# Kernel tuning notes

Hardware: AMD Instinct MI355X
Metric: run time of the kernel (lower is better)

Reference implementation:

```python
import jax, jax.numpy as jnp
import numpy as np

D_MODEL = 768
NUM_HEADS = 12
D_HEAD = D_MODEL // NUM_HEADS


def setup_inputs() -> dict:
    key = jax.random.key(0)
    ks = jax.random.split(key, 11)
    B, S = 1, 4096
    s = 1.0 / np.sqrt(D_MODEL)
    inp = {
        'q': jax.random.normal(ks[0], (B, S, D_MODEL), dtype=jnp.float32),
        'k': jax.random.normal(ks[1], (B, S, D_MODEL), dtype=jnp.float32),
        'v': jax.random.normal(ks[2], (B, S, D_MODEL), dtype=jnp.float32),
        'wq': jax.random.normal(ks[3], (D_MODEL, D_MODEL), dtype=jnp.float32) * s,
        'bq': jnp.zeros((D_MODEL,), dtype=jnp.float32),
        'wk': jax.random.normal(ks[4], (D_MODEL, D_MODEL), dtype=jnp.float32) * s,
        'bk': jnp.zeros((D_MODEL,), dtype=jnp.float32),
        'wv': jax.random.normal(ks[5], (D_MODEL, D_MODEL), dtype=jnp.float32) * s,
        'bv': jnp.zeros((D_MODEL,), dtype=jnp.float32),
        'wo': jax.random.normal(ks[6], (D_MODEL, D_MODEL), dtype=jnp.float32) * s,
        'bo': jnp.zeros((D_MODEL,), dtype=jnp.float32),
    }
    return inp


def reference(q, k, v, wq, bq, wk, bk, wv, bv, wo, bo):
    B, S, _ = q.shape
    # linear projections (torch Linear: x @ W^T + b)
    qh = (q @ wq.T + bq).reshape(B, S, NUM_HEADS, D_HEAD).transpose(0, 2, 1, 3)
    kh = (k @ wk.T + bk).reshape(B, S, NUM_HEADS, D_HEAD).transpose(0, 2, 1, 3)
    vh = (v @ wv.T + bv).reshape(B, S, NUM_HEADS, D_HEAD).transpose(0, 2, 1, 3)
    scores = jnp.einsum('bhqd,bhkd->bhqk', qh, kh) / jnp.sqrt(jnp.float32(D_HEAD))
    causal = jnp.tril(jnp.ones((S, S), dtype=bool))  # [S,S] causal mask
    scores = jnp.where(causal, scores, jnp.finfo(scores.dtype).min)
    attn = jax.nn.softmax(scores, axis=-1)  # dropout omitted (eval mode)
    out = jnp.einsum('bhqk,bhkd->bhqd', attn, vh)
    out = out.transpose(0, 2, 1, 3).reshape(B, S, D_MODEL)
    return out @ wo.T + bo
```

## Files before the change

### kernel.cpp

```cpp
#include <hip/hip_runtime.h>
#include <stdint.h>

typedef __attribute__((ext_vector_type(8))) short short8;
typedef __attribute__((ext_vector_type(4))) short short4v;
typedef __attribute__((ext_vector_type(4))) float float4v;
typedef __attribute__((ext_vector_type(2))) uint32_t uint32x2;
typedef __attribute__((ext_vector_type(4))) uint32_t uint32x4;

__device__ __forceinline__ unsigned short f2bf(float f) {
  union { float f; uint32_t u; } v;
  v.f = f;
  uint32_t u = v.u;
  return (unsigned short)((u + 0x7fffu + ((u >> 16) & 1u)) >> 16);
}

__device__ __forceinline__ uint32_t pkbf(float a, float b) {
#if __has_builtin(__builtin_amdgcn_cvt_pk_bf16_f32)
  typedef __attribute__((ext_vector_type(2))) __bf16 bf16x2;
  bf16x2 r = __builtin_amdgcn_cvt_pk_bf16_f32(a, b);
  union { bf16x2 v; uint32_t u; } c;
  c.v = r;
  return c.u;
#else
  return (uint32_t)f2bf(a) | ((uint32_t)f2bf(b) << 16);
#endif
}

__device__ __forceinline__ float fexp2(float x) {
#if __has_builtin(__builtin_amdgcn_exp2f)
  return __builtin_amdgcn_exp2f(x);
#else
  return exp2f(x);
#endif
}

__device__ __forceinline__ float4v mfma16bf(short4v a, short4v b, float4v c) {
#if __has_builtin(__builtin_amdgcn_mfma_f32_16x16x16bf16_1k)
  return __builtin_amdgcn_mfma_f32_16x16x16bf16_1k(a, b, c, 0, 0, 0);
#else
  float4v d;
  asm("v_mfma_f32_16x16x16_bf16 %0, %1, %2, %3"
      : "=v"(d) : "v"(a), "v"(b), "v"(c));
  return d;
#endif
}

__device__ __forceinline__ void gll16(const unsigned short* g, unsigned short* l) {
  __builtin_amdgcn_global_load_lds(
      (const __attribute__((address_space(1))) void*)g,
      (__attribute__((address_space(3))) void*)l, 16, 0, 0);
}

struct CvtArgs {
  const float* src[4];
  unsigned short* dst[4];
};

__global__ __launch_bounds__(256) void cvt_all(CvtArgs a) {
  const int bid = blockIdx.x;
  const int t = bid / 288, off = bid - t * 288;
  const size_t i = (size_t)off * 256 + threadIdx.x;
  const float4v* p = (const float4v*)(a.src[t] + i * 8);
  float4v x = p[0], y = p[1];
  uint32x4 o;
  o[0] = pkbf(x[0], x[1]);
  o[1] = pkbf(x[2], x[3]);
  o[2] = pkbf(y[0], y[1]);
  o[3] = pkbf(y[2], y[3]);
  *(uint32x4*)(a.dst[t] + i * 8) = o;
}

__global__ __launch_bounds__(256) void gemm_qkv(
    const float* __restrict__ xq, const float* __restrict__ xk,
    const float* __restrict__ xv,
    const unsigned short* __restrict__ wqb, const unsigned short* __restrict__ wkb,
    const unsigned short* __restrict__ wvb,
    const float* __restrict__ bq, const float* __restrict__ bk,
    const float* __restrict__ bv,
    unsigned short* __restrict__ Qp, unsigned short* __restrict__ Kp,
    unsigned short* __restrict__ Vt, float qscale)
{
  __shared__ unsigned short As[128 * 64];
  __shared__ unsigned short Ws[128 * 64];
  const int z = blockIdx.z;
  const float* A32 = z == 0 ? xq : z == 1 ? xk : xv;
  const unsigned short* W = z == 0 ? wqb : z == 1 ? wkb : wvb;
  const float* bias = z == 0 ? bq : z == 1 ? bk : bv;
  const int M = 4096, N = 768, K = 768;
  const int tid = threadIdx.x, wave = tid >> 6, lane = tid & 63;
  const int g = lane >> 4, l16 = lane & 15;
  const int sw = l16 & 7;
  const int m0 = blockIdx.x * 128, n0 = blockIdx.y * 128;
  const int wn = (wave >> 1) * 64, wm = (wave & 1) * 64;
  const int srow0 = wave * 32 + (lane >> 3);
  const int skg = lane & 7;

  float4v acc[4][4] = {};

  for (int k0 = 0; k0 < K; k0 += 64) {
    if (k0) __syncthreads();
    #pragma unroll
    for (int c = 0; c < 4; ++c) {
      const int row = srow0 + c * 8;
      const int kg = skg ^ (row & 7);
      gll16(W + (size_t)(n0 + row) * K + k0 + kg * 8, &Ws[(wave * 32 + c * 8) * 64]);
    }
    #pragma unroll
    for (int inst = 0; inst < 8; ++inst) {
      const int f = inst * 256 + tid;
      const int row = f >> 4, c = f & 15;
      float4v a = *(const float4v*)(A32 + (size_t)(m0 + row) * K + k0 + c * 4);
      uint32x2 pk;
      pk[0] = pkbf(a[0], a[1]);
      pk[1] = pkbf(a[2], a[3]);
      const int s = c >> 1;
      *(uint32x2*)&As[row * 64 + ((s ^ (row & 7)) * 8) + (c & 1) * 4] = pk;
    }
    __syncthreads();
    #pragma unroll
    for (int kk = 0; kk < 2; ++kk) {
      const int kg = ((kk * 4 + g) ^ sw) * 8;
      short8 xf[4], wf[4];
      #pragma unroll
      for (int t = 0; t < 4; ++t) {
        xf[t] = *(const short8*)&As[(wm + t * 16 + l16) * 64 + kg];
        wf[t] = *(const short8*)&Ws[(wn + t * 16 + l16) * 64 + kg];
      }
      if (z < 2) {
        #pragma unroll
        for (int i = 0; i < 4; ++i)
          #pragma unroll
          for (int j = 0; j < 4; ++j)
            acc[i][j] = __builtin_amdgcn_mfma_f32_16x16x32_bf16(wf[i], xf[j], acc[i][j], 0, 0, 0);
      } else {
        #pragma unroll
        for (int i = 0; i < 4; ++i)
          #pragma unroll
          for (int j = 0; j < 4; ++j)
            acc[i][j] = __builtin_amdgcn_mfma_f32_16x16x32_bf16(xf[i], wf[j], acc[i][j], 0, 0, 0);
      }
    }
  }

  if (z < 2) {
    unsigned short* O = z == 0 ? Qp : Kp;
    const float osc = z == 0 ? qscale : 1.0f;
    #pragma unroll
    for (int i = 0; i < 4; ++i) {
      const int nb = n0 + wn + i * 16 + 4 * g;
      const float4v bb = *(const float4v*)&bias[nb];
      #pragma unroll
      for (int j = 0; j < 4; ++j) {
        const int m = m0 + wm + j * 16 + l16;
        uint32x2 pk;
        pk[0] = pkbf((acc[i][j][0] + bb[0]) * osc, (acc[i][j][1] + bb[1]) * osc);
        pk[1] = pkbf((acc[i][j][2] + bb[2]) * osc, (acc[i][j][3] + bb[3]) * osc);
        *(uint32x2*)(O + (size_t)m * N + nb) = pk;
      }
    }
  } else {
    #pragma unroll
    for (int j = 0; j < 4; ++j) {
      const int n = n0 + wn + j * 16 + l16;
      const float bb = bias[n];
      #pragma unroll
      for (int i = 0; i < 4; ++i) {
        const int mb = m0 + wm + i * 16 + 4 * g;
        uint32x2 pk;
        pk[0] = pkbf(acc[i][j][0] + bb, acc[i][j][1] + bb);
        pk[1] = pkbf(acc[i][j][2] + bb, acc[i][j][3] + bb);
        *(uint32x2*)(Vt + (size_t)n * M + mb) = pk;
      }
    }
  }
}

__global__ __launch_bounds__(256, 4) void flash_part(
    const unsigned short* __restrict__ Qp,
    const unsigned short* __restrict__ Kp,
    const unsigned short* __restrict__ Vt,
    unsigned short* __restrict__ Opart,
    float* __restrict__ lpart)
{
  __shared__ unsigned short lds_k[2][64 * 64];
  __shared__ unsigned short lds_v[2][64 * 64];
  const int S = 4096, DM = 768;

  const int gid = blockIdx.x;
  const int h = gid % 12;
  const int e = 79 - gid / 12;
  int t, c;
  if (e < 8)       { t = e;                c = 0; }
  else if (e < 24) { t = 8 + (e - 8) / 2;  c = (e - 8) % 2; }
  else if (e < 48) { t = 16 + (e - 24) / 3; c = (e - 24) % 3; }
  else             { t = 24 + (e - 48) / 4; c = (e - 48) % 4; }
  const int kb0 = c * 16;
  const int kbe = min(kb0 + 16, 2 * t + 2);

  const int tid = threadIdx.x, wave = tid >> 6, lane = tid & 63;
  const int g = lane >> 4, l16 = lane & 15;
  const int sw = l16 & 7;
  const int qbase = t * 128 + wave * 32;

  short8 qf[2][2];
  #pragma unroll
  for (int qc = 0; qc < 2; ++qc) {
    const unsigned short* qp = Qp + (size_t)(qbase + qc * 16 + l16) * DM + h * 64;
    qf[qc][0] = *(const short8*)(qp + g * 8);
    qf[qc][1] = *(const short8*)(qp + 32 + g * 8);
  }

  float4v o[2][4] = {};
  float lsum[2] = {0.0f, 0.0f};

  const int strow = wave * 16 + (lane >> 3);
  const int skg = lane & 7;

  #pragma unroll
  for (int cc = 0; cc < 2; ++cc) {
    const int row = strow + cc * 8;
    const int kg = skg ^ (row & 7);
    gll16(Kp + (size_t)(kb0 * 64 + row) * DM + h * 64 + kg * 8,
          &lds_k[0][(wave * 16 + cc * 8) * 64]);
    gll16(Vt + (size_t)(h * 64 + row) * S + kb0 * 64 + kg * 8,
          &lds_v[0][(wave * 16 + cc * 8) * 64]);
  }
  __syncthreads();

  for (int kb = kb0; kb < kbe; ++kb) {
    const int cur = kb & 1;
    if (kb + 1 < kbe) {
      const int nb = cur ^ 1;
      #pragma unroll
      for (int cc = 0; cc < 2; ++cc) {
        const int row = strow + cc * 8;
        const int kg = skg ^ (row & 7);
        gll16(Kp + (size_t)((kb + 1) * 64 + row) * DM + h * 64 + kg * 8,
              &lds_k[nb][(wave * 16 + cc * 8) * 64]);
        gll16(Vt + (size_t)(h * 64 + row) * S + (kb + 1) * 64 + kg * 8,
              &lds_v[nb][(wave * 16 + cc * 8) * 64]);
      }
    }
    const unsigned short* kc = lds_k[cur];
    const unsigned short* vc = lds_v[cur];

    float4v sf[2][4];
    #pragma unroll
    for (int mt = 0; mt < 4; ++mt) {
      short8 ka0 = *(const short8*)&kc[(mt * 16 + l16) * 64 + ((0 + g) ^ sw) * 8];
      short8 ka1 = *(const short8*)&kc[(mt * 16 + l16) * 64 + ((4 + g) ^ sw) * 8];
      #pragma unroll
      for (int qc = 0; qc < 2; ++qc) {
        float4v a = {};
        a = __builtin_amdgcn_mfma_f32_16x16x32_bf16(ka0, qf[qc][0], a, 0, 0, 0);
        a = __builtin_amdgcn_mfma_f32_16x16x32_bf16(ka1, qf[qc][1], a, 0, 0, 0);
        sf[qc][mt] = a;
      }
    }

    if ((kb + 1) * 64 > qbase) {
      #pragma unroll
      for (int qc = 0; qc < 2; ++qc) {
        const int q = qbase + qc * 16 + l16;
        #pragma unroll
        for (int mt = 0; mt < 4; ++mt)
          #pragma unroll
          for (int rr = 0; rr < 4; ++rr) {
            const int key = kb * 64 + mt * 16 + 4 * g + rr;
            sf[qc][mt][rr] = (key <= q) ? sf[qc][mt][rr] : -1e30f;
          }
      }
    }

    short4v pb[2][4];
    #pragma unroll
    for (int qc = 0; qc < 2; ++qc)
      #pragma unroll
      for (int mt = 0; mt < 4; ++mt) {
        float4v pe;
        #pragma unroll
        for (int rr = 0; rr < 4; ++rr) {
          pe[rr] = fexp2(sf[qc][mt][rr]);
          lsum[qc] += pe[rr];
        }
        union { uint32x2 u; short4v s; } cv;
        cv.u[0] = pkbf(pe[0], pe[1]);
        cv.u[1] = pkbf(pe[2], pe[3]);
        pb[qc][mt] = cv.s;
      }

    #pragma unroll
    for (int ms = 0; ms < 4; ++ms) {
      const int slot = ((2 * ms + (g >> 1)) ^ sw) * 8 + (g & 1) * 4;
      #pragma unroll
      for (int dt = 0; dt < 4; ++dt) {
        short4v va = *(const short4v*)&vc[(dt * 16 + l16) * 64 + slot];
        o[0][dt] = mfma16bf(va, pb[0][ms], o[0][dt]);
        o[1][dt] = mfma16bf(va, pb[1][ms], o[1][dt]);
      }
    }

    __syncthreads();
  }

  const int slot = (h * 32 + t) * 4 + c;
  unsigned short* ob = Opart + (size_t)slot * 8192;
  #pragma unroll
  for (int qc = 0; qc < 2; ++qc) {
    float L = lsum[qc];
    L += __shfl_xor(L, 16);
    L += __shfl_xor(L, 32);
    const int ql = wave * 32 + qc * 16 + l16;
    if (g == 0) lpart[slot * 128 + ql] = L;
    #pragma unroll
    for (int dt = 0; dt < 4; ++dt) {
      uint32x2 ov;
      ov[0] = pkbf(o[qc][dt][0], o[qc][dt][1]);
      ov[1] = pkbf(o[qc][dt][2], o[qc][dt][3]);
      *(uint32x2*)(ob + (size_t)ql * 64 + dt * 16 + 4 * g) = ov;
    }
  }
}

__global__ __launch_bounds__(256) void flash_combine(
    const unsigned short* __restrict__ Opart, const float* __restrict__ lpart,
    unsigned short* __restrict__ AO)
{
  const int t = blockIdx.x, h = blockIdx.y;
  const int nc = (2 * t + 17) >> 4;
  const int slot0 = (h * 32 + t) * 4;
  const int tid = threadIdx.x;
  const int qr = tid >> 2, dc = (tid & 3) * 16;
  #pragma unroll
  for (int it = 0; it < 2; ++it) {
    const int ql = it * 64 + qr;
    float acc[16];
    #pragma unroll
    for (int j = 0; j < 16; ++j) acc[j] = 0.0f;
    float lsum = 0.0f;
    for (int cc = 0; cc < nc; ++cc) {
      const int slot = slot0 + cc;
      lsum += lpart[slot * 128 + ql];
      const uint32x4* p = (const uint32x4*)(Opart + (size_t)slot * 8192 + ql * 64 + dc);
      uint32x4 w0 = p[0], w1 = p[1];
      #pragma unroll
      for (int j = 0; j < 4; ++j) {
        union { uint32_t u; float f; } lo, hi;
        lo.u = w0[j] << 16; hi.u = w0[j] & 0xffff0000u;
        acc[2 * j] += lo.f; acc[2 * j + 1] += hi.f;
        lo.u = w1[j] << 16; hi.u = w1[j] & 0xffff0000u;
        acc[8 + 2 * j] += lo.f; acc[8 + 2 * j + 1] += hi.f;
      }
    }
    const float inv = 1.0f / lsum;
    uint32x4 o0, o1;
    #pragma unroll
    for (int j = 0; j < 4; ++j) {
      o0[j] = pkbf(acc[2 * j] * inv, acc[2 * j + 1] * inv);
      o1[j] = pkbf(acc[8 + 2 * j] * inv, acc[8 + 2 * j + 1] * inv);
    }
    unsigned short* dst = AO + (size_t)(t * 128 + ql) * 768 + h * 64 + dc;
    *(uint32x4*)dst = o0;
    *(uint32x4*)(dst + 8) = o1;
  }
}

__global__ __launch_bounds__(256) void gemm_out(
    const unsigned short* __restrict__ A, const unsigned short* __restrict__ W,
    const float* __restrict__ bias, float* __restrict__ Out)
{
  __shared__ unsigned short As[128 * 64];
  __shared__ unsigned short Ws[128 * 64];
  const int N = 768, K = 768;
  const int tid = threadIdx.x, wave = tid >> 6, lane = tid & 63;
  const int g = lane >> 4, l16 = lane & 15;
  const int sw = l16 & 7;
  const int m0 = blockIdx.x * 128, n0 = blockIdx.y * 128;
  const int wn = (wave >> 1) * 64, wm = (wave & 1) * 64;
  const int srow0 = wave * 32 + (lane >> 3);
  const int skg = lane & 7;

  float4v acc[4][4] = {};

  for (int k0 = 0; k0 < K; k0 += 64) {
    if (k0) __syncthreads();
    #pragma unroll
    for (int c = 0; c < 4; ++c) {
      const int row = srow0 + c * 8;
      const int kg = skg ^ (row & 7);
      gll16(A + (size_t)(m0 + row) * K + k0 + kg * 8, &As[(wave * 32 + c * 8) * 64]);
      gll16(W + (size_t)(n0 + row) * K + k0 + kg * 8, &Ws[(wave * 32 + c * 8) * 64]);
    }
    __syncthreads();
    #pragma unroll
    for (int kk = 0; kk < 2; ++kk) {
      const int kg = ((kk * 4 + g) ^ sw) * 8;
      short8 xf[4], wf[4];
      #pragma unroll
      for (int t = 0; t < 4; ++t) {
        xf[t] = *(const short8*)&As[(wm + t * 16 + l16) * 64 + kg];
        wf[t] = *(const short8*)&Ws[(wn + t * 16 + l16) * 64 + kg];
      }
      #pragma unroll
      for (int i = 0; i < 4; ++i)
        #pragma unroll
        for (int j = 0; j < 4; ++j)
          acc[i][j] = __builtin_amdgcn_mfma_f32_16x16x32_bf16(wf[i], xf[j], acc[i][j], 0, 0, 0);
    }
  }

  #pragma unroll
  for (int i = 0; i < 4; ++i) {
    const int nb = n0 + wn + i * 16 + 4 * g;
    const float4v bb = *(const float4v*)&bias[nb];
    #pragma unroll
    for (int j = 0; j < 4; ++j) {
      const int m = m0 + wm + j * 16 + l16;
      float4v ov;
      #pragma unroll
      for (int rr = 0; rr < 4; ++rr) ov[rr] = acc[i][j][rr] + bb[rr];
      *(float4v*)(Out + (size_t)m * N + nb) = ov;
    }
  }
}

extern "C" void kernel_launch(void* const* d_in, const int* in_sizes, int n_in,
                              void* d_out, int out_size, void* d_ws, size_t ws_size,
                              hipStream_t stream) {
  const float* q  = (const float*)d_in[0];
  const float* k  = (const float*)d_in[1];
  const float* v  = (const float*)d_in[2];
  const float* wq = (const float*)d_in[3];
  const float* bq = (const float*)d_in[4];
  const float* wk = (const float*)d_in[5];
  const float* bk = (const float*)d_in[6];
  const float* wv = (const float*)d_in[7];
  const float* bv = (const float*)d_in[8];
  const float* wo = (const float*)d_in[9];
  const float* bo = (const float*)d_in[10];
  float* out = (float*)d_out;

  const int S = 4096, D = 768;
  unsigned short* Qp    = (unsigned short*)d_ws;
  unsigned short* Kp    = Qp  + (size_t)S * D;
  unsigned short* Vt    = Kp  + (size_t)S * D;
  unsigned short* AO    = Vt  + (size_t)S * D;
  unsigned short* wqb   = AO  + (size_t)S * D;
  unsigned short* wkb   = wqb + (size_t)D * D;
  unsigned short* wvb   = wkb + (size_t)D * D;
  unsigned short* wob   = wvb + (size_t)D * D;
  unsigned short* Opart = wob + (size_t)D * D;
  float*          lpart = (float*)(Opart + (size_t)1536 * 8192);

  CvtArgs ca;
  ca.src[0] = wq; ca.dst[0] = wqb;
  ca.src[1] = wk; ca.dst[1] = wkb;
  ca.src[2] = wv; ca.dst[2] = wvb;
  ca.src[3] = wo; ca.dst[3] = wob;

  const float SC = 0.125f * 1.44269504089f;
  dim3 blk(256);
  cvt_all<<<dim3(1152), blk, 0, stream>>>(ca);
  gemm_qkv<<<dim3(32, 6, 3), blk, 0, stream>>>(q, k, v, wqb, wkb, wvb,
                                               bq, bk, bv, Qp, Kp, Vt, SC);
  flash_part<<<dim3(960), blk, 0, stream>>>(Qp, Kp, Vt, Opart, lpart);
  flash_combine<<<dim3(32, 12), blk, 0, stream>>>(Opart, lpart, AO);
  gemm_out<<<dim3(32, 6), blk, 0, stream>>>(AO, wob, bo, out);
}
```

Baseline: 217.1 us.

## Triple-buffer K tiles with partial vmcnt barriers and remap flash block order

The flash attention kernel now prefetches K two tiles ahead using a third LDS buffer, and V one tile ahead. Barriers use explicit s_waitcnt on vmcnt so only the oldest loads must finish before each sync, letting newer prefetches stay in flight. The grid-to-(head, work item) mapping is also reordered, grouping blocks eight heads at a time and pairing the remaining four heads. The extra LDS buffer may lower occupancy, and the hand-coded waitcnt values depend on the exact number of loads issued per iteration.

```diff
diff --git a/kernel.cpp b/kernel.cpp
--- a/kernel.cpp
+++ b/kernel.cpp
@@ -49,6 +49,15 @@
   __builtin_amdgcn_global_load_lds(
       (const __attribute__((address_space(1))) void*)g,
       (__attribute__((address_space(3))) void*)l, 16, 0, 0);
+}
+
+__device__ __forceinline__ void barrier_vm2() {
+  __builtin_amdgcn_s_waitcnt(0x0F72);
+  __builtin_amdgcn_s_barrier();
+}
+__device__ __forceinline__ void barrier_vm0() {
+  __builtin_amdgcn_s_waitcnt(0x0F70);
+  __builtin_amdgcn_s_barrier();
 }
 
 struct CvtArgs {
@@ -182,16 +191,18 @@
     unsigned short* __restrict__ Opart,
     float* __restrict__ lpart)
 {
-  __shared__ unsigned short lds_k[2][64 * 64];
+  __shared__ unsigned short lds_k[3][64 * 64];
   __shared__ unsigned short lds_v[2][64 * 64];
   const int S = 4096, DM = 768;
 
   const int gid = blockIdx.x;
-  const int h = gid % 12;
-  const int e = 79 - gid / 12;
+  const int x = gid & 7, j = gid >> 3;
+  int h, e;
+  if (j < 80) { h = x; e = j; }
+  else        { h = 8 + (x >> 1); e = 2 * (j - 80) + (x & 1); }
   int t, c;
-  if (e < 8)       { t = e;                c = 0; }
-  else if (e < 24) { t = 8 + (e - 8) / 2;  c = (e - 8) % 2; }
+  if (e < 8)       { t = e;                 c = 0; }
+  else if (e < 24) { t = 8 + (e - 8) / 2;   c = (e - 8) % 2; }
   else if (e < 48) { t = 16 + (e - 24) / 3; c = (e - 24) % 3; }
   else             { t = 24 + (e - 48) / 4; c = (e - 48) % 4; }
   const int kb0 = c * 16;
@@ -215,40 +226,56 @@
 
   const int strow = wave * 16 + (lane >> 3);
   const int skg = lane & 7;
+  const int ldso = (wave * 16) * 64;
+
+  unsigned short* k0 = lds_k[0];
+  unsigned short* k1 = lds_k[1];
+  unsigned short* k2 = lds_k[2];
+  unsigned short* v0 = lds_v[0];
+  unsigned short* v1 = lds_v[1];
 
   #pragma unroll
   for (int cc = 0; cc < 2; ++cc) {
     const int row = strow + cc * 8;
     const int kg = skg ^ (row & 7);
-    gll16(Kp + (size_t)(kb0 * 64 + row) * DM + h * 64 + kg * 8,
-          &lds_k[0][(wave * 16 + cc * 8) * 64]);
-    gll16(Vt + (size_t)(h * 64 + row) * S + kb0 * 64 + kg * 8,
-          &lds_v[0][(wave * 16 + cc * 8) * 64]);
-  }
-  __syncthreads();
+    gll16(Kp + (size_t)(kb0 * 64 + row) * DM + h * 64 + kg * 8, k0 + ldso + cc * 512);
+    gll16(Vt + (size_t)(h * 64 + row) * S + kb0 * 64 + kg * 8,  v0 + ldso + cc * 512);
+  }
+  #pragma unroll
+  for (int cc = 0; cc < 2; ++cc) {
+    const int row = strow + cc * 8;
+    const int kg = skg ^ (row & 7);
+    gll16(Kp + (size_t)((kb0 + 1) * 64 + row) * DM + h * 64 + kg * 8, k1 + ldso + cc * 512);
+  }
+  barrier_vm2();
 
   for (int kb = kb0; kb < kbe; ++kb) {
-    const int cur = kb & 1;
-    if (kb + 1 < kbe) {
-      const int nb = cur ^ 1;
+    const bool nv = (kb + 1 < kbe);
+    const bool nk = (kb + 2 < kbe);
+    if (nv) {
       #pragma unroll
       for (int cc = 0; cc < 2; ++cc) {
         const int row = strow + cc * 8;
         const int kg = skg ^ (row & 7);
-        gll16(Kp + (size_t)((kb + 1) * 64 + row) * DM + h * 64 + kg * 8,
-              &lds_k[nb][(wave * 16 + cc * 8) * 64]);
         gll16(Vt + (size_t)(h * 64 + row) * S + (kb + 1) * 64 + kg * 8,
-              &lds_v[nb][(wave * 16 + cc * 8) * 64]);
-      }
-    }
-    const unsigned short* kc = lds_k[cur];
-    const unsigned short* vc = lds_v[cur];
+              v1 + ldso + cc * 512);
+      }
+    }
+    if (nk) {
+      #pragma unroll
+      for (int cc = 0; cc < 2; ++cc) {
+        const int row = strow + cc * 8;
+        const int kg = skg ^ (row & 7);
+        gll16(Kp + (size_t)((kb + 2) * 64 + row) * DM + h * 64 + kg * 8,
+              k2 + ldso + cc * 512);
+      }
+    }
 
     float4v sf[2][4];
     #pragma unroll
     for (int mt = 0; mt < 4; ++mt) {
-      short8 ka0 = *(const short8*)&kc[(mt * 16 + l16) * 64 + ((0 + g) ^ sw) * 8];
-      short8 ka1 = *(const short8*)&kc[(mt * 16 + l16) * 64 + ((4 + g) ^ sw) * 8];
+      short8 ka0 = *(const short8*)&k0[(mt * 16 + l16) * 64 + ((0 + g) ^ sw) * 8];
+      short8 ka1 = *(const short8*)&k0[(mt * 16 + l16) * 64 + ((4 + g) ^ sw) * 8];
       #pragma unroll
       for (int qc = 0; qc < 2; ++qc) {
         float4v a = {};
@@ -294,13 +321,18 @@
       const int slot = ((2 * ms + (g >> 1)) ^ sw) * 8 + (g & 1) * 4;
       #pragma unroll
       for (int dt = 0; dt < 4; ++dt) {
-        short4v va = *(const short4v*)&vc[(dt * 16 + l16) * 64 + slot];
+        short4v va = *(const short4v*)&v0[(dt * 16 + l16) * 64 + slot];
         o[0][dt] = mfma16bf(va, pb[0][ms], o[0][dt]);
         o[1][dt] = mfma16bf(va, pb[1][ms], o[1][dt]);
       }
     }
 
-    __syncthreads();
+    if (nv) {
+      if (nk) barrier_vm2();
+      else    barrier_vm0();
+    }
+    unsigned short* tk = k0; k0 = k1; k1 = k2; k2 = tk;
+    unsigned short* tv = v0; v0 = v1; v1 = tv;
   }
 
   const int slot = (h * 32 + t) * 4 + c;
```

Result: no change. 219.1 us (+0.9%).
